# Kernel tuning notes

Hardware: AMD Instinct MI355X
Metric: run time of the kernel (lower is better)

The kernel has to match this reference:

```python
import jax, jax.numpy as jnp
import numpy as np

N_CLASSES = 91


def setup_inputs() -> dict:
    key = jax.random.key(0)
    k1, k2 = jax.random.split(key)
    shape = (64, 512, 512)
    inputs = jax.random.randint(k1, shape, 0, N_CLASSES).astype(jnp.float32)
    targets = jax.random.randint(k2, shape, 0, N_CLASSES).astype(jnp.int32)
    return {"inputs": inputs, "targets": targets, "smooth": 1}


def reference(inputs, targets, smooth):
    # Single-pass confusion-histogram formulation of the per-class IoU loop.
    x = inputs.reshape(-1).astype(jnp.int32)   # predicted class ids
    t = targets.reshape(-1).astype(jnp.int32)  # target class ids
    # per-class counts: a_cnt[i] = sum(inputs==i), b_cnt[i] = sum(targets==i)
    a_cnt = jnp.bincount(x, length=N_CLASSES).astype(jnp.float32)
    b_cnt = jnp.bincount(t, length=N_CLASSES).astype(jnp.float32)
    # intersection[i] = sum((inputs==i) & (targets==i)); route mismatches to bin N_CLASSES
    inter = jnp.bincount(jnp.where(x == t, x, N_CLASSES), length=N_CLASSES + 1)[:N_CLASSES].astype(jnp.float32)
    union = a_cnt + b_cnt - inter
    valid = union != 0
    smooth_f = jnp.float32(smooth)
    iou = (inter + smooth_f) / (union + smooth_f)
    sum_iou = jnp.sum(jnp.where(valid, iou, jnp.float32(0)))
    num_classes = jnp.sum(valid).astype(jnp.float32)
    return sum_iou / num_classes
```

## Files before the change

### kernel.cpp

```cpp
#include <hip/hip_runtime.h>

#define N_CLASSES 91
#define NBINS (3 * N_CLASSES)
#define HPAD (N_CLASSES + 1)

__global__ void miou_zero_ws(unsigned int* __restrict__ ws) {
    int i = threadIdx.x + blockIdx.x * blockDim.x;
    if (i < NBINS) ws[i] = 0u;
}

__global__ __launch_bounds__(256) void miou_hist(const float* __restrict__ inp,
                                                 const int* __restrict__ tgt,
                                                 unsigned int* __restrict__ ws,
                                                 int n4) {
    __shared__ unsigned int h[4][3][HPAD];
    const int wave = threadIdx.x >> 6;

    for (int i = threadIdx.x; i < 4 * 3 * HPAD; i += blockDim.x)
        ((unsigned int*)h)[i] = 0u;
    __syncthreads();

    const int stride = gridDim.x * blockDim.x;
    for (int idx = blockIdx.x * blockDim.x + threadIdx.x; idx < n4; idx += stride) {
        const float4 f = reinterpret_cast<const float4*>(inp)[idx];
        const int4  t = reinterpret_cast<const int4*>(tgt)[idx];
        const int x0 = (int)f.x, x1 = (int)f.y, x2 = (int)f.z, x3 = (int)f.w;

        atomicAdd(&h[wave][0][x0], 1u);
        atomicAdd(&h[wave][0][x1], 1u);
        atomicAdd(&h[wave][0][x2], 1u);
        atomicAdd(&h[wave][0][x3], 1u);

        atomicAdd(&h[wave][1][t.x], 1u);
        atomicAdd(&h[wave][1][t.y], 1u);
        atomicAdd(&h[wave][1][t.z], 1u);
        atomicAdd(&h[wave][1][t.w], 1u);

        if (x0 == t.x) atomicAdd(&h[wave][2][x0], 1u);
        if (x1 == t.y) atomicAdd(&h[wave][2][x1], 1u);
        if (x2 == t.z) atomicAdd(&h[wave][2][x2], 1u);
        if (x3 == t.w) atomicAdd(&h[wave][2][x3], 1u);
    }
    __syncthreads();

    for (int i = threadIdx.x; i < NBINS; i += blockDim.x) {
        const int arr = i / N_CLASSES;
        const int c   = i - arr * N_CLASSES;
        const unsigned int s = h[0][arr][c] + h[1][arr][c] + h[2][arr][c] + h[3][arr][c];
        if (s) atomicAdd(&ws[i], s);
    }
}

__global__ __launch_bounds__(128) void miou_finalize(const unsigned int* __restrict__ ws,
                                                     const int* __restrict__ smooth,
                                                     float* __restrict__ out) {
    const int c = threadIdx.x;
    float s = 0.f, cnt = 0.f;
    if (c < N_CLASSES) {
        const float a     = (float)ws[c];
        const float b     = (float)ws[N_CLASSES + c];
        const float inter = (float)ws[2 * N_CLASSES + c];
        const float uni   = a + b - inter;
        if (uni != 0.f) {
            const float sm = (float)(*smooth);
            s   = (inter + sm) / (uni + sm);
            cnt = 1.f;
        }
    }
    #pragma unroll
    for (int off = 32; off > 0; off >>= 1) {
        s   += __shfl_down(s, off, 64);
        cnt += __shfl_down(cnt, off, 64);
    }
    __shared__ float ssum[2], scnt[2];
    const int wave = threadIdx.x >> 6;
    const int lane = threadIdx.x & 63;
    if (lane == 0) { ssum[wave] = s; scnt[wave] = cnt; }
    __syncthreads();
    if (threadIdx.x == 0) {
        const float tot = ssum[0] + ssum[1];
        const float n   = scnt[0] + scnt[1];
        out[0] = tot / n;
    }
}

extern "C" void kernel_launch(void* const* d_in, const int* in_sizes, int n_in,
                              void* d_out, int out_size, void* d_ws, size_t ws_size,
                              hipStream_t stream) {
    const float* inp   = (const float*)d_in[0];
    const int*   tgt   = (const int*)d_in[1];
    const int*   smooth = (const int*)d_in[2];
    float* out = (float*)d_out;
    unsigned int* ws = (unsigned int*)d_ws;

    const int n  = in_sizes[0];
    const int n4 = n >> 2;

    miou_zero_ws<<<1, 512, 0, stream>>>(ws);

    const int block = 256;
    int grid = (n4 + block - 1) / block;
    if (grid > 2048) grid = 2048;
    miou_hist<<<grid, block, 0, stream>>>(inp, tgt, ws, n4);

    miou_finalize<<<1, 128, 0, stream>>>(ws, smooth, out);
}
```

Before: 174.9 us.

## Replicate shared histogram 32 ways per lane and fuse finalize via last-block pattern

Replaces the per-wave shared histograms with a 32-column replicated layout indexed by lane, so lanes of a wave hitting the same class land in distinct LDS banks and addresses, reducing atomic contention and serialization. Per-bin reduction sums the 32 columns with a rotated index to avoid bank conflicts. The separate finalize kernel is removed; the last block to finish, detected through an atomic counter plus threadfence, computes the IoU mean. This costs about 35KB of LDS per block, which may lower occupancy, and adds a grid-wide counter.

```diff
diff --git a/kernel.cpp b/kernel.cpp
--- a/kernel.cpp
+++ b/kernel.cpp
@@ -2,93 +2,97 @@
 
 #define N_CLASSES 91
 #define NBINS (3 * N_CLASSES)
-#define HPAD (N_CLASSES + 1)
+#define HCOLS 32
+#define HSIZE (NBINS * HCOLS)
 
 __global__ void miou_zero_ws(unsigned int* __restrict__ ws) {
-    int i = threadIdx.x + blockIdx.x * blockDim.x;
-    if (i < NBINS) ws[i] = 0u;
+    int i = threadIdx.x;
+    if (i < NBINS + 1) ws[i] = 0u;
 }
 
 __global__ __launch_bounds__(256) void miou_hist(const float* __restrict__ inp,
                                                  const int* __restrict__ tgt,
                                                  unsigned int* __restrict__ ws,
+                                                 const int* __restrict__ smooth,
+                                                 float* __restrict__ out,
                                                  int n4) {
-    __shared__ unsigned int h[4][3][HPAD];
-    const int wave = threadIdx.x >> 6;
+    __shared__ unsigned int h[HSIZE];
+    const int tid = threadIdx.x;
+    const int col = tid & 31;
 
-    for (int i = threadIdx.x; i < 4 * 3 * HPAD; i += blockDim.x)
-        ((unsigned int*)h)[i] = 0u;
+    for (int i = tid; i < HSIZE; i += 256) h[i] = 0u;
     __syncthreads();
 
     const int stride = gridDim.x * blockDim.x;
-    for (int idx = blockIdx.x * blockDim.x + threadIdx.x; idx < n4; idx += stride) {
+    for (int idx = blockIdx.x * blockDim.x + tid; idx < n4; idx += stride) {
         const float4 f = reinterpret_cast<const float4*>(inp)[idx];
         const int4  t = reinterpret_cast<const int4*>(tgt)[idx];
         const int x0 = (int)f.x, x1 = (int)f.y, x2 = (int)f.z, x3 = (int)f.w;
 
-        atomicAdd(&h[wave][0][x0], 1u);
-        atomicAdd(&h[wave][0][x1], 1u);
-        atomicAdd(&h[wave][0][x2], 1u);
-        atomicAdd(&h[wave][0][x3], 1u);
+        atomicAdd(&h[x0 * HCOLS + col], 1u);
+        atomicAdd(&h[x1 * HCOLS + col], 1u);
+        atomicAdd(&h[x2 * HCOLS + col], 1u);
+        atomicAdd(&h[x3 * HCOLS + col], 1u);
 
-        atomicAdd(&h[wave][1][t.x], 1u);
-        atomicAdd(&h[wave][1][t.y], 1u);
-        atomicAdd(&h[wave][1][t.z], 1u);
-        atomicAdd(&h[wave][1][t.w], 1u);
+        atomicAdd(&h[(N_CLASSES + t.x) * HCOLS + col], 1u);
+        atomicAdd(&h[(N_CLASSES + t.y) * HCOLS + col], 1u);
+        atomicAdd(&h[(N_CLASSES + t.z) * HCOLS + col], 1u);
+        atomicAdd(&h[(N_CLASSES + t.w) * HCOLS + col], 1u);
 
-        if (x0 == t.x) atomicAdd(&h[wave][2][x0], 1u);
-        if (x1 == t.y) atomicAdd(&h[wave][2][x1], 1u);
-        if (x2 == t.z) atomicAdd(&h[wave][2][x2], 1u);
-        if (x3 == t.w) atomicAdd(&h[wave][2][x3], 1u);
+        if (x0 == t.x) atomicAdd(&h[(2 * N_CLASSES + x0) * HCOLS + col], 1u);
+        if (x1 == t.y) atomicAdd(&h[(2 * N_CLASSES + x1) * HCOLS + col], 1u);
+        if (x2 == t.z) atomicAdd(&h[(2 * N_CLASSES + x2) * HCOLS + col], 1u);
+        if (x3 == t.w) atomicAdd(&h[(2 * N_CLASSES + x3) * HCOLS + col], 1u);
     }
     __syncthreads();
 
-    for (int i = threadIdx.x; i < NBINS; i += blockDim.x) {
-        const int arr = i / N_CLASSES;
-        const int c   = i - arr * N_CLASSES;
-        const unsigned int s = h[0][arr][c] + h[1][arr][c] + h[2][arr][c] + h[3][arr][c];
+    for (int i = tid; i < NBINS; i += 256) {
+        unsigned int s = 0;
+        const int base = i * HCOLS;
+        #pragma unroll
+        for (int k = 0; k < HCOLS; ++k) s += h[base + ((k + tid) & 31)];
         if (s) atomicAdd(&ws[i], s);
     }
-}
+    __threadfence();
 
-__global__ __launch_bounds__(128) void miou_finalize(const unsigned int* __restrict__ ws,
-                                                     const int* __restrict__ smooth,
-                                                     float* __restrict__ out) {
-    const int c = threadIdx.x;
-    float s = 0.f, cnt = 0.f;
-    if (c < N_CLASSES) {
-        const float a     = (float)ws[c];
-        const float b     = (float)ws[N_CLASSES + c];
-        const float inter = (float)ws[2 * N_CLASSES + c];
-        const float uni   = a + b - inter;
-        if (uni != 0.f) {
-            const float sm = (float)(*smooth);
-            s   = (inter + sm) / (uni + sm);
-            cnt = 1.f;
+    __shared__ unsigned int lastflag;
+    if (tid == 0) {
+        const unsigned int old = atomicAdd(&ws[NBINS], 1u);
+        lastflag = (old == (unsigned int)gridDim.x - 1u) ? 1u : 0u;
+    }
+    __syncthreads();
+    if (lastflag) {
+        float s = 0.f, cnt = 0.f;
+        if (tid < N_CLASSES) {
+            const float a     = (float)atomicAdd(&ws[tid], 0u);
+            const float b     = (float)atomicAdd(&ws[N_CLASSES + tid], 0u);
+            const float inter = (float)atomicAdd(&ws[2 * N_CLASSES + tid], 0u);
+            const float uni   = a + b - inter;
+            if (uni != 0.f) {
+                const float sm = (float)(*smooth);
+                s   = (inter + sm) / (uni + sm);
+                cnt = 1.f;
+            }
         }
-    }
-    #pragma unroll
-    for (int off = 32; off > 0; off >>= 1) {
-        s   += __shfl_down(s, off, 64);
-        cnt += __shfl_down(cnt, off, 64);
-    }
-    __shared__ float ssum[2], scnt[2];
-    const int wave = threadIdx.x >> 6;
-    const int lane = threadIdx.x & 63;
-    if (lane == 0) { ssum[wave] = s; scnt[wave] = cnt; }
-    __syncthreads();
-    if (threadIdx.x == 0) {
-        const float tot = ssum[0] + ssum[1];
-        const float n   = scnt[0] + scnt[1];
-        out[0] = tot / n;
+        #pragma unroll
+        for (int off = 32; off > 0; off >>= 1) {
+            s   += __shfl_down(s, off, 64);
+            cnt += __shfl_down(cnt, off, 64);
+        }
+        __shared__ float rs[4], rc[4];
+        const int w = tid >> 6;
+        if ((tid & 63) == 0) { rs[w] = s; rc[w] = cnt; }
+        __syncthreads();
+        if (tid == 0) out[0] = (rs[0] + rs[1] + rs[2] + rs[3]) /
+                               (rc[0] + rc[1] + rc[2] + rc[3]);
     }
 }
 
 extern "C" void kernel_launch(void* const* d_in, const int* in_sizes, int n_in,
                               void* d_out, int out_size, void* d_ws, size_t ws_size,
                               hipStream_t stream) {
-    const float* inp   = (const float*)d_in[0];
-    const int*   tgt   = (const int*)d_in[1];
+    const float* inp    = (const float*)d_in[0];
+    const int*   tgt    = (const int*)d_in[1];
     const int*   smooth = (const int*)d_in[2];
     float* out = (float*)d_out;
     unsigned int* ws = (unsigned int*)d_ws;
@@ -101,7 +105,5 @@
     const int block = 256;
     int grid = (n4 + block - 1) / block;
     if (grid > 2048) grid = 2048;
-    miou_hist<<<grid, block, 0, stream>>>(inp, tgt, ws, n4);
-
-    miou_finalize<<<1, 128, 0, stream>>>(ws, smooth, out);
+    miou_hist<<<grid, block, 0, stream>>>(inp, tgt, ws, smooth, out, n4);
 }
```

New measurement: 295.8 us. 1.69x slower.
